# Kernel optimization log

Hardware: AMD Instinct MI355X
Metric: run time of the kernel (lower is better)

## Reference

```python
import jax, jax.numpy as jnp
import numpy as np

EPS = 1e-6
POSE_W, DEPTH_W, POINTS_W, NORMAL_W = 1.0, 1.0, 1.0, 0.1
DEPTH_MIN = 1e-6


def mat_to_quat(M):
    # pytorch3d-style robust rotation-matrix -> quaternion (w,x,y,z)
    m00, m01, m02 = M[..., 0, 0], M[..., 0, 1], M[..., 0, 2]
    m10, m11, m12 = M[..., 1, 0], M[..., 1, 1], M[..., 1, 2]
    m20, m21, m22 = M[..., 2, 0], M[..., 2, 1], M[..., 2, 2]
    q_abs = jnp.sqrt(jnp.maximum(jnp.stack([
        1.0 + m00 + m11 + m22,
        1.0 + m00 - m11 - m22,
        1.0 - m00 + m11 - m22,
        1.0 - m00 - m11 + m22], axis=-1), 0.0))
    cand = jnp.stack([
        jnp.stack([q_abs[..., 0] ** 2, m21 - m12, m02 - m20, m10 - m01], -1),
        jnp.stack([m21 - m12, q_abs[..., 1] ** 2, m10 + m01, m02 + m20], -1),
        jnp.stack([m02 - m20, m10 + m01, q_abs[..., 2] ** 2, m12 + m21], -1),
        jnp.stack([m10 - m01, m20 + m02, m21 + m12, q_abs[..., 3] ** 2], -1),
    ], axis=-2)  # [...,4,4]
    cand = cand / (2.0 * jnp.maximum(q_abs[..., None], 0.1))
    best = jnp.argmax(q_abs, axis=-1)
    quat = jnp.take_along_axis(cand, best[..., None, None], axis=-2)[..., 0, :]
    return jnp.where(quat[..., 0:1] < 0, -quat, quat)


def pose_encoding(extri, intr, H, W):
    # extri [B,S,3,4] -> [B,S,9] = absT(3) + quat(4) + fov_h,fov_w
    T = extri[..., :3, 3]
    quat = mat_to_quat(extri[..., :3, :3])
    fov_h = 2.0 * jnp.arctan((H / 2.0) / intr[..., 1, 1])
    fov_w = 2.0 * jnp.arctan((W / 2.0) / intr[..., 0, 0])
    return jnp.concatenate([T, quat, fov_h[..., None], fov_w[..., None]], axis=-1)


def align_depth_scale(dp, dg, vm):
    # batched masked-median scale; dp detached by caller. Returns (aligned_gt, scales[B,S])
    B, S, H, W = dg.shape
    dpf, dgf = dp.reshape(B, S, H * W), dg.reshape(B, S, H * W)
    m = vm.reshape(B, S, H * W)
    m2 = m & jnp.isfinite(dpf) & (dpf > EPS)
    ratio = dpf / jnp.maximum(dgf, EPS)
    fm = m2 & jnp.isfinite(ratio)
    msum = m2.sum(-1)
    fcnt = fm.sum(-1)
    r = jnp.sort(jnp.where(fm, ratio, jnp.inf), axis=-1)
    idx = jnp.maximum((fcnt - 1) // 2, 0)  # torch lower median
    med = jnp.take_along_axis(r, idx[..., None], axis=-1)[..., 0]
    scale = jnp.clip(med, 1e-3, 1e3)
    scale = jnp.where((msum < 16) | (fcnt == 0), jnp.ones_like(scale), scale)
    return dg * scale[..., None, None], scale


def _cam_grid(depth, intr):
    B, S, H, W = depth.shape
    ys, xs = jnp.meshgrid(jnp.arange(H, dtype=depth.dtype),
                          jnp.arange(W, dtype=depth.dtype), indexing='ij')
    fx = intr[..., 0, 0][..., None, None]
    fy = intr[..., 1, 1][..., None, None]
    cx = intr[..., 0, 2][..., None, None]
    cy = intr[..., 1, 2][..., None, None]
    x = (xs - cx) / jnp.maximum(fx, EPS) * depth
    y = (ys - cy) / jnp.maximum(fy, EPS) * depth
    return jnp.stack([x, y, depth], axis=-1)  # [B,S,H,W,3]


def depth_to_normals(depth, intr):
    pts = _cam_grid(depth, intr)
    fx_diff = pts[..., 1:-1, 2:, :] - pts[..., 1:-1, :-2, :]
    fy_diff = pts[..., 2:, 1:-1, :] - pts[..., :-2, 1:-1, :]
    core = jnp.cross(fy_diff, fx_diff)
    core = core / jnp.maximum(jnp.linalg.norm(core, axis=-1, keepdims=True), EPS)
    return jnp.zeros_like(pts).at[..., 1:-1, 1:-1, :].set(core)


def depth_to_world_points(depth, intr, pose):
    cam_pts = _cam_grid(depth, intr)
    rot = pose[..., :3, :3]
    trans = pose[..., :3, 3]
    return jnp.einsum('bsij,bshwj->bshwi', rot, cam_pts) + trans[..., None, None, :]


def masked_l1(pred, target, mask):
    mask = mask.astype(pred.dtype)
    return ((pred - target) * mask).__abs__().sum() / jnp.maximum(mask.sum(), 1.0)


def masked_cosine_loss(pred, target, mask):
    pred = pred / jnp.maximum(jnp.linalg.norm(pred, axis=-1, keepdims=True), EPS)
    target = target / jnp.maximum(jnp.linalg.norm(target, axis=-1, keepdims=True), EPS)
    cos = jnp.clip((pred * target).sum(-1), -1.0, 1.0)
    m = mask.astype(cos.dtype)
    return ((1.0 - cos) * m).sum() / jnp.maximum(m.sum(), 1.0)


def smooth_l1(pred, target):
    d = jnp.abs(pred - target)
    return jnp.mean(jnp.where(d < 1.0, 0.5 * d * d, d - 0.5))


def supervised_loss(depth_pred, points_pred, pose_pred, depth_gt, intrinsics,
                    pose_matrix_gt, valid_mask):
    B, S, H, W = depth_gt.shape
    vm = valid_mask & jnp.isfinite(depth_gt) & (depth_gt > DEPTH_MIN)
    depth_gt_aligned, scales = align_depth_scale(
        jax.lax.stop_gradient(depth_pred), depth_gt, vm)
    points_gt = depth_to_world_points(depth_gt_aligned, intrinsics, pose_matrix_gt)
    points_mask = jnp.broadcast_to(vm[..., None], points_gt.shape)
    # normal mask: zero-out 1-pixel border
    border = jnp.zeros((H, W), dtype=bool).at[1:-1, 1:-1].set(True)
    normal_mask = vm & border
    pred_normals = depth_to_normals(depth_pred, intrinsics)
    gt_normals = depth_to_normals(depth_gt, intrinsics)
    normal_loss = masked_cosine_loss(pred_normals, gt_normals, normal_mask)
    pose_gt = pose_encoding(pose_matrix_gt[..., :3, :], intrinsics, H, W)
    pose_gt = pose_gt.at[..., :3].multiply(scales[..., None])
    depth_loss = masked_l1(depth_pred, depth_gt_aligned, vm)
    points_loss = masked_l1(points_pred, points_gt, points_mask)
    pose_loss = smooth_l1(pose_pred, pose_gt)
    return (POSE_W * pose_loss + DEPTH_W * depth_loss
            + POINTS_W * points_loss + NORMAL_W * normal_loss)


def setup_inputs() -> dict:
    key = jax.random.key(0)
    ks = jax.random.split(key, 7)
    B, S, H, W = 4, 8, 384, 512
    depth_gt = jax.random.uniform(ks[0], (B, S, H, W), minval=0.5, maxval=10.0)
    depth_pred = depth_gt * jax.random.uniform(ks[1], (B, S, H, W), minval=0.8, maxval=1.2)
    points_pred = jax.random.normal(ks[2], (B, S, H, W, 3))
    pose_pred = 0.1 * jax.random.normal(ks[3], (B, S, 9))
    intr = jnp.broadcast_to(jnp.array([[500.0, 0.0, W / 2.0],
                                       [0.0, 500.0, H / 2.0],
                                       [0.0, 0.0, 1.0]], jnp.float32), (B, S, 3, 3))
    q, _ = jnp.linalg.qr(jax.random.normal(ks[4], (B, S, 3, 3)))
    R = q * jnp.sign(jnp.linalg.det(q))[..., None, None]  # det=+1
    t = jax.random.normal(ks[5], (B, S, 3))
    top = jnp.concatenate([R, t[..., None]], axis=-1)
    bottom = jnp.broadcast_to(jnp.array([0.0, 0.0, 0.0, 1.0], jnp.float32), (B, S, 1, 4))
    pose_matrix_gt = jnp.concatenate([top, bottom], axis=-2)
    valid_mask = jax.random.uniform(ks[6], (B, S, H, W)) > 0.05
    return {"depth_pred": depth_pred, "points_pred": points_pred,
            "pose_pred": pose_pred, "depth_gt": depth_gt,
            "intrinsics": intr, "pose_matrix_gt": pose_matrix_gt,
            "valid_mask": valid_mask}


def reference(depth_pred, points_pred, pose_pred, depth_gt, intrinsics,
              pose_matrix_gt, valid_mask):
    return supervised_loss(depth_pred, points_pred, pose_pred, depth_gt,
                           intrinsics, pose_matrix_gt, valid_mask)
```

## Files before the change

kernel.cpp:

```cpp
#include <hip/hip_runtime.h>
#include <stdint.h>

#define H_ 384
#define W_ 512
#define HW_ (H_ * W_)
#define NIMG 32
#define EPSF 1e-6f
#define HBLK 16
#define HTHR 512
#define PXB (HW_ / HBLK)
#define CITER (PXB / (HTHR * 4))
#define NPARTS (HBLK * NIMG)
#define SENT 0xFFFFFFFFu

#define OFF_MSUM   0
#define OFF_FCNT   32
#define OFF_KREM1  64
#define OFF_PREF1  96
#define OFF_SCALE  128
#define OFF_POSE   160
#define OFF_PMF    192
#define OFF_PART   1216
#define OFF_PHA    3776
#define OFF_PHB    (OFF_PHA + NIMG*HBLK*2048)

__device__ __forceinline__ bool finitef(float x) {
    return ((__float_as_uint(x) >> 23) & 0xFFu) != 0xFFu;
}

__global__ __launch_bounds__(HTHR) void hist0_k(
    const float* __restrict__ dp, const float* __restrict__ dg,
    const uint8_t* __restrict__ vmask, uint32_t* __restrict__ ws)
{
    __shared__ uint32_t lh[2048];
    __shared__ int sm[8], sf[8];
    const int img = blockIdx.y, blk = blockIdx.x, t = threadIdx.x;
    for (int b = t; b < 2048; b += HTHR) lh[b] = 0;
    __syncthreads();

    const size_t base = (size_t)img * HW_;
    const float* dpi = dp + base;
    const float* dgi = dg + base;
    const uint8_t* mi = vmask + base;

    int m2c = 0, fmc = 0;

    for (int c = 0; c < CITER; ++c) {
        const int pix = blk * PXB + c * (HTHR * 4) + t * 4;
        const float4 v_dp = *reinterpret_cast<const float4*>(dpi + pix);
        const float4 v_dg = *reinterpret_cast<const float4*>(dgi + pix);
        const uchar4 v_m  = *reinterpret_cast<const uchar4*>(mi + pix);
        const float dpa[4] = {v_dp.x, v_dp.y, v_dp.z, v_dp.w};
        const float dga[4] = {v_dg.x, v_dg.y, v_dg.z, v_dg.w};
        const uint8_t ma[4] = {v_m.x, v_m.y, v_m.z, v_m.w};
        int bins[4]; bool fms[4];
#pragma unroll
        for (int e = 0; e < 4; ++e) {
            const float dgv = dga[e], dpv = dpa[e];
            const bool vm = ma[e] && finitef(dgv) && (dgv > 1e-6f);
            const bool m2 = vm && finitef(dpv) && (dpv > EPSF);
            const float ratio = dpv / fmaxf(dgv, EPSF);
            const bool fm = m2 && finitef(ratio);
            m2c += (int)m2; fmc += (int)fm;
            const uint32_t key = fm ? __float_as_uint(ratio) : SENT;
            bins[e] = (int)(key >> 21);
            fms[e] = fm;
        }

#pragma unroll
        for (int e = 0; e < 4; ++e) {
            const bool fm = fms[e];
            const int bin = bins[e];
            unsigned long long todo = __ballot(fm);
            while (todo) {
                const int lead = (int)__ffsll(todo) - 1;
                const int lbin = __shfl(bin, lead);
                const unsigned long long same = __ballot(fm && (bin == lbin));
                if ((t & 63) == lead)
                    atomicAdd(&lh[lbin], (uint32_t)__popcll(same));
                todo &= ~same;
            }
        }
    }

    for (int o = 32; o > 0; o >>= 1) { m2c += __shfl_down(m2c, o); fmc += __shfl_down(fmc, o); }
    if ((t & 63) == 0) { sm[t >> 6] = m2c; sf[t >> 6] = fmc; }
    __syncthreads();
    if (t == 0) {
        int M = 0, F = 0;
        for (int w = 0; w < 8; ++w) { M += sm[w]; F += sf[w]; }
        int* pmf = (int*)(ws + OFF_PMF) + (img * HBLK + blk) * 2;
        pmf[0] = M; pmf[1] = F;
    }

    uint32_t* phb = ws + OFF_PHA + (size_t)(img * HBLK + blk) * 2048;
    for (int b = t; b < 2048; b += HTHR) phb[b] = lh[b];
}

__global__ __launch_bounds__(HTHR) void histp1_k(
    const float* __restrict__ dp, const float* __restrict__ dg,
    const uint8_t* __restrict__ vmask, uint32_t* __restrict__ ws)
{
    __shared__ uint32_t lh[2048];
    __shared__ uint32_t wsum[8];
    __shared__ int s_bin, s_krem, s_msum, s_fcnt;
    const int img = blockIdx.y, blk = blockIdx.x, t = threadIdx.x;

    const uint32_t* pin = ws + OFF_PHA + (size_t)img * HBLK * 2048;
    uint32_t local[4];
#pragma unroll
    for (int c = 0; c < 4; ++c) local[c] = 0;
    for (int b = 0; b < HBLK; ++b) {
        const uint32_t* row = pin + b * 2048 + t * 4;
#pragma unroll
        for (int c = 0; c < 4; ++c) local[c] += row[c];
    }
    const uint32_t cs = local[0] + local[1] + local[2] + local[3];

    uint32_t v = cs;
#pragma unroll
    for (int o = 1; o < 64; o <<= 1) {
        const uint32_t u = __shfl_up(v, o);
        if ((t & 63) >= o) v += u;
    }
    if ((t & 63) == 63) wsum[t >> 6] = v;
    if (t == 0) {
        s_bin = 0; s_krem = 0;
        const int* pmf = (const int*)(ws + OFF_PMF) + img * HBLK * 2;
        int M = 0, F = 0;
        for (int b = 0; b < HBLK; ++b) { M += pmf[2 * b]; F += pmf[2 * b + 1]; }
        s_msum = M; s_fcnt = F;
    }
    __syncthreads();
    uint32_t woff = 0;
    for (int w = 0; w < (t >> 6); ++w) woff += wsum[w];
    const uint32_t incl = woff + v;
    const uint32_t excl = incl - cs;

    const uint32_t k = (uint32_t)max((s_fcnt - 1) / 2, 0);
    if (k >= excl && k < incl) {
        uint32_t cum = excl;
#pragma unroll
        for (int c = 0; c < 4; ++c) {
            if (cum + local[c] > k) { s_bin = t * 4 + c; s_krem = (int)(k - cum); break; }
            cum += local[c];
        }
    }
    __syncthreads();
    if (t == 0 && blk == 0) {
        ((int*)(ws + OFF_MSUM))[img] = s_msum;
        ((int*)(ws + OFF_FCNT))[img] = s_fcnt;
        (ws + OFF_PREF1)[img] = (uint32_t)s_bin << 21;
        ((int*)(ws + OFF_KREM1))[img] = s_krem;
    }
    const uint32_t pm = (uint32_t)s_bin;

    for (int b = t; b < 2048; b += HTHR) lh[b] = 0;
    __syncthreads();

    const size_t base = (size_t)img * HW_;
    for (int c = 0; c < CITER; ++c) {
        const int pix = blk * PXB + c * (HTHR * 4) + t * 4;
        const float4 v_dp = *reinterpret_cast<const float4*>(dp + base + pix);
        const float4 v_dg = *reinterpret_cast<const float4*>(dg + base + pix);
        const uchar4 v_m  = *reinterpret_cast<const uchar4*>(vmask + base + pix);
        const float dpa[4] = {v_dp.x, v_dp.y, v_dp.z, v_dp.w};
        const float dga[4] = {v_dg.x, v_dg.y, v_dg.z, v_dg.w};
        const uint8_t ma[4] = {v_m.x, v_m.y, v_m.z, v_m.w};
#pragma unroll
        for (int e = 0; e < 4; ++e) {
            const float dgv = dga[e], dpv = dpa[e];
            const bool vm = ma[e] && finitef(dgv) && (dgv > 1e-6f);
            const bool m2 = vm && finitef(dpv) && (dpv > EPSF);
            const float ratio = dpv / fmaxf(dgv, EPSF);
            const bool fm = m2 && finitef(ratio);
            const uint32_t key = fm ? __float_as_uint(ratio) : SENT;
            if ((key >> 21) == pm)
                atomicAdd(&lh[(key >> 10) & 2047u], 1u);
        }
    }
    __syncthreads();

    uint32_t* pout = ws + OFF_PHB + (size_t)(img * HBLK + blk) * 2048;
    for (int b = t; b < 2048; b += HTHR) pout[b] = lh[b];
}

__global__ __launch_bounds__(256) void sel_mid_k(
    uint32_t* __restrict__ ws,
    const float* __restrict__ intr, const float* __restrict__ posegt,
    const float* __restrict__ posepred)
{
    const int img = blockIdx.x;
    const int t = threadIdx.x;
    const uint32_t* ph = ws + OFF_PHB + (size_t)img * HBLK * 2048;
    uint32_t local[8];
#pragma unroll
    for (int c = 0; c < 8; ++c) local[c] = 0;
    for (int b = 0; b < HBLK; ++b) {
        const uint32_t* row = ph + b * 2048 + t * 8;
#pragma unroll
        for (int c = 0; c < 8; ++c) local[c] += row[c];
    }
    uint32_t cs = 0;
#pragma unroll
    for (int c = 0; c < 8; ++c) cs += local[c];

    __shared__ uint32_t wsum[4];
    __shared__ int s_bin;
    uint32_t v = cs;
#pragma unroll
    for (int o = 1; o < 64; o <<= 1) {
        const uint32_t u = __shfl_up(v, o);
        if ((t & 63) >= o) v += u;
    }
    if ((t & 63) == 63) wsum[t >> 6] = v;
    if (t == 0) s_bin = 0;
    __syncthreads();
    uint32_t woff = 0;
    for (int w = 0; w < (t >> 6); ++w) woff += wsum[w];
    const uint32_t incl = woff + v;
    const uint32_t excl = incl - cs;

    const uint32_t k = (uint32_t)((const int*)(ws + OFF_KREM1))[img];
    if (k >= excl && k < incl) {
        uint32_t cum = excl;
#pragma unroll
        for (int c = 0; c < 8; ++c) {
            if (cum + local[c] > k) { s_bin = t * 8 + c; break; }
            cum += local[c];
        }
    }
    __syncthreads();

    if (t == 0) {
        const uint32_t med_u = (ws + OFF_PREF1)[img] | ((uint32_t)s_bin << 10) | 512u;
        const float med = __uint_as_float(med_u);
        float sc_ = fminf(fmaxf(med, 0.001f), 1000.0f);
        const int fcnt = ((const int*)(ws + OFF_FCNT))[img];
        const int msum = ((const int*)(ws + OFF_MSUM))[img];
        if (msum < 16 || fcnt == 0) sc_ = 1.0f;
        ((float*)(ws + OFF_SCALE))[img] = sc_;

        const float* p = posegt + img * 16;
        const float m00 = p[0], m01 = p[1], m02 = p[2], tx = p[3];
        const float m10 = p[4], m11 = p[5], m12 = p[6], ty = p[7];
        const float m20 = p[8], m21 = p[9], m22 = p[10], tz = p[11];
        float qa[4];
        qa[0] = sqrtf(fmaxf(1.0f + m00 + m11 + m22, 0.0f));
        qa[1] = sqrtf(fmaxf(1.0f + m00 - m11 - m22, 0.0f));
        qa[2] = sqrtf(fmaxf(1.0f - m00 + m11 - m22, 0.0f));
        qa[3] = sqrtf(fmaxf(1.0f - m00 - m11 + m22, 0.0f));
        int best = 0; float bv = qa[0];
        for (int i2 = 1; i2 < 4; ++i2) if (qa[i2] > bv) { bv = qa[i2]; best = i2; }
        float c0, c1, c2, c3;
        if (best == 0)      { c0 = qa[0]*qa[0]; c1 = m21 - m12;   c2 = m02 - m20;   c3 = m10 - m01; }
        else if (best == 1) { c0 = m21 - m12;   c1 = qa[1]*qa[1]; c2 = m10 + m01;   c3 = m02 + m20; }
        else if (best == 2) { c0 = m02 - m20;   c1 = m10 + m01;   c2 = qa[2]*qa[2]; c3 = m12 + m21; }
        else                { c0 = m10 - m01;   c1 = m20 + m02;   c2 = m21 + m12;   c3 = qa[3]*qa[3]; }
        const float denom = 2.0f * fmaxf(qa[best], 0.1f);
        float q0 = c0 / denom, q1 = c1 / denom, q2 = c2 / denom, q3 = c3 / denom;
        if (q0 < 0.0f) { q0 = -q0; q1 = -q1; q2 = -q2; q3 = -q3; }
        const float fx = intr[img * 9 + 0], fy = intr[img * 9 + 4];
        const float fovh = 2.0f * atanf((H_ * 0.5f) / fy);
        const float fovw = 2.0f * atanf((W_ * 0.5f) / fx);
        const float pg[9] = {tx * sc_, ty * sc_, tz * sc_, q0, q1, q2, q3, fovh, fovw};
        const float* ppred = posepred + img * 9;
        float s = 0.0f;
        for (int i2 = 0; i2 < 9; ++i2) {
            const float d = fabsf(ppred[i2] - pg[i2]);
            s += (d < 1.0f) ? 0.5f * d * d : d - 0.5f;
        }
        ((float*)(ws + OFF_POSE))[img] = s;
    }
}

__global__ __launch_bounds__(HTHR) void main_loss(
    const float* __restrict__ dp, const float* __restrict__ dg,
    const uint8_t* __restrict__ vmask, const float* __restrict__ pts_pred,
    const float* __restrict__ intr, const float* __restrict__ posegt,
    uint32_t* __restrict__ ws)
{
    const int img = blockIdx.y, blk = blockIdx.x, t = threadIdx.x;
    __shared__ float sP[17];
    if (t == 0) {
        const float* p = posegt + img * 16;
        sP[0] = p[0]; sP[1] = p[1]; sP[2] = p[2];  sP[9]  = p[3];
        sP[3] = p[4]; sP[4] = p[5]; sP[5] = p[6];  sP[10] = p[7];
        sP[6] = p[8]; sP[7] = p[9]; sP[8] = p[10]; sP[11] = p[11];
        sP[12] = intr[img * 9 + 0]; sP[13] = intr[img * 9 + 4];
        sP[14] = intr[img * 9 + 2]; sP[15] = intr[img * 9 + 5];
        sP[16] = ((const float*)(ws + OFF_SCALE))[img];
    }
    __syncthreads();
    const float R00 = sP[0], R01 = sP[1], R02 = sP[2];
    const float R10 = sP[3], R11 = sP[4], R12 = sP[5];
    const float R20 = sP[6], R21 = sP[7], R22 = sP[8];
    const float T0 = sP[9], T1 = sP[10], T2 = sP[11];
    const float inv_fx = 1.0f / fmaxf(sP[12], EPSF);
    const float inv_fy = 1.0f / fmaxf(sP[13], EPSF);
    const float cx = sP[14], cy = sP[15];
    const float sc = sP[16];

    const size_t base = (size_t)img * HW_;
    const float* dpi = dp + base;
    const float* dgi = dg + base;

    float dsum = 0.0f, psum = 0.0f, nsum = 0.0f;
    float vcnt = 0.0f, ncnt = 0.0f;

    for (int c = 0; c < CITER; ++c) {
        const int pix = blk * PXB + c * (HTHR * 4) + t * 4;
        const int i = pix >> 9;
        const int j0 = pix & 511;

        const float4 v_dp = *reinterpret_cast<const float4*>(dpi + pix);
        const float4 v_dg = *reinterpret_cast<const float4*>(dgi + pix);
        const uchar4 v_m  = *reinterpret_cast<const uchar4*>(vmask + base + pix);
        const float4 pp0 = *reinterpret_cast<const float4*>(pts_pred + (base + pix) * 3);
        const float4 pp1 = *reinterpret_cast<const float4*>(pts_pred + (base + pix) * 3 + 4);
        const float4 pp2 = *reinterpret_cast<const float4*>(pts_pred + (base + pix) * 3 + 8);

        const int im = (i > 0) ? i - 1 : 0;
        const int ip = (i < H_ - 1) ? i + 1 : i;
        const int jme = (j0 > 0) ? j0 - 1 : 0;
        const int jpe = (j0 + 4 < W_) ? j0 + 4 : W_ - 1;
        const float4 dpU = *reinterpret_cast<const float4*>(dpi + im * W_ + j0);
        const float4 dpD = *reinterpret_cast<const float4*>(dpi + ip * W_ + j0);
        const float4 dgU = *reinterpret_cast<const float4*>(dgi + im * W_ + j0);
        const float4 dgD = *reinterpret_cast<const float4*>(dgi + ip * W_ + j0);
        const float dpLe = dpi[i * W_ + jme], dpRe = dpi[i * W_ + jpe];
        const float dgLe = dgi[i * W_ + jme], dgRe = dgi[i * W_ + jpe];

        const float ppv[12] = {pp0.x, pp0.y, pp0.z, pp0.w, pp1.x, pp1.y, pp1.z, pp1.w,
                               pp2.x, pp2.y, pp2.z, pp2.w};
        const float dpa[4] = {v_dp.x, v_dp.y, v_dp.z, v_dp.w};
        const float dga[4] = {v_dg.x, v_dg.y, v_dg.z, v_dg.w};
        const float dpUa[4] = {dpU.x, dpU.y, dpU.z, dpU.w};
        const float dpDa[4] = {dpD.x, dpD.y, dpD.z, dpD.w};
        const float dgUa[4] = {dgU.x, dgU.y, dgU.z, dgU.w};
        const float dgDa[4] = {dgD.x, dgD.y, dgD.z, dgD.w};
        const uint8_t ma[4] = {v_m.x, v_m.y, v_m.z, v_m.w};

        const float ay = ((float)i - cy) * inv_fy;
        const bool row_int = (i >= 1) && (i <= H_ - 2);

#pragma unroll
        for (int e = 0; e < 4; ++e) {
            const int j = j0 + e;
            const float dgv = dga[e], dpv = dpa[e];
            const bool vm = ma[e] && finitef(dgv) && (dgv > 1e-6f);
            const bool nm = vm && row_int && (j >= 1) && (j <= W_ - 2);
            vcnt += vm ? 1.0f : 0.0f;
            ncnt += nm ? 1.0f : 0.0f;

            const float dal = dgv * sc;
            dsum += vm ? fabsf(dpv - dal) : 0.0f;
            const float ax = ((float)j - cx) * inv_fx;
            const float cxx = ax * dal, cyy = ay * dal;
            const float wx = R00 * cxx + R01 * cyy + R02 * dal + T0;
            const float wy = R10 * cxx + R11 * cyy + R12 * dal + T1;
            const float wz = R20 * cxx + R21 * cyy + R22 * dal + T2;
            const float pl = fabsf(ppv[3 * e] - wx) + fabsf(ppv[3 * e + 1] - wy)
                           + fabsf(ppv[3 * e + 2] - wz);
            psum += vm ? pl : 0.0f;

            const float pdL = (e == 0) ? dpLe : dpa[e - 1];
            const float pdR = (e == 3) ? dpRe : dpa[e + 1];
            const float gdL = (e == 0) ? dgLe : dga[e - 1];
            const float gdR = (e == 3) ? dgRe : dga[e + 1];
            const float pdU = dpUa[e], pdD = dpDa[e];
            const float gdU = dgUa[e], gdD = dgDa[e];

            const float dRLp = pdR - pdL, dDUp = pdD - pdU;
            const float Ap = inv_fy * (pdD + pdU);
            const float Bp = inv_fx * (pdR + pdL);
            const float cpx = dRLp * Ap;
            const float cpy = dDUp * Bp;
            const float cpz = -(Ap * Bp + ax * cpx + ay * cpy);
            const float dRLg = gdR - gdL, dDUg = gdD - gdU;
            const float Ag = inv_fy * (gdD + gdU);
            const float Bg = inv_fx * (gdR + gdL);
            const float cgx = dRLg * Ag;
            const float cgy = dDUg * Bg;
            const float cgz = -(Ag * Bg + ax * cgx + ay * cgy);

            const float np2 = cpx * cpx + cpy * cpy + cpz * cpz;
            const float ng2 = cgx * cgx + cgy * cgy + cgz * cgz;
            const float dpg = cpx * cgx + cpy * cgy + cpz * cgz;
            const float den = fmaxf(np2, 1e-12f) * fmaxf(ng2, 1e-12f);
            float cosv = dpg * __builtin_amdgcn_rsqf(den);
            cosv = fminf(fmaxf(cosv, -1.0f), 1.0f);
            nsum += nm ? (1.0f - cosv) : 0.0f;
        }
    }

    float vals[5] = {vcnt, dsum, psum, nsum, ncnt};
    __shared__ float red[8][5];
    const int wave = t >> 6, lane = t & 63;
#pragma unroll
    for (int q = 0; q < 5; ++q) {
        float v = vals[q];
        for (int o = 32; o > 0; o >>= 1) v += __shfl_down(v, o);
        if (lane == 0) red[wave][q] = v;
    }
    __syncthreads();
    if (t == 0) {
        const int slot = img * HBLK + blk;
        float* part = (float*)(ws + OFF_PART) + slot * 5;
#pragma unroll
        for (int q = 0; q < 5; ++q) {
            float s = 0.0f;
            for (int w = 0; w < 8; ++w) s += red[w][q];
            part[q] = s;
        }
    }
}

__global__ __launch_bounds__(256) void finalize_k(const uint32_t* __restrict__ ws,
                                                  float* __restrict__ out)
{
    const float* part = (const float*)(ws + OFF_PART);
    const int t = threadIdx.x;
    double s[5] = {0, 0, 0, 0, 0};
    for (int slot = t; slot < NPARTS; slot += 256) {
#pragma unroll
        for (int q = 0; q < 5; ++q) s[q] += (double)part[slot * 5 + q];
    }
    __shared__ double red[4][5];
    const int wave = t >> 6, lane = t & 63;
#pragma unroll
    for (int q = 0; q < 5; ++q) {
        double v = s[q];
        for (int o = 32; o > 0; o >>= 1) v += __shfl_down(v, o);
        if (lane == 0) red[wave][q] = v;
    }
    __syncthreads();
    if (t == 0) {
        double tot[5];
#pragma unroll
        for (int q = 0; q < 5; ++q)
            tot[q] = red[0][q] + red[1][q] + red[2][q] + red[3][q];
        const float* pose = (const float*)(ws + OFF_POSE);
        double ps = 0.0;
        for (int i2 = 0; i2 < NIMG; ++i2) ps += (double)pose[i2];
        const double vmc = tot[0];
        const double depth_loss  = tot[1] / fmax(vmc, 1.0);
        const double points_loss = tot[2] / fmax(3.0 * vmc, 1.0);
        const double normal_loss = tot[3] / fmax(tot[4], 1.0);
        const double pose_loss   = ps / 288.0;
        out[0] = (float)(pose_loss + depth_loss + points_loss + 0.1 * normal_loss);
    }
}

extern "C" void kernel_launch(void* const* d_in, const int* in_sizes, int n_in,
                              void* d_out, int out_size, void* d_ws, size_t ws_size,
                              hipStream_t stream)
{
    const float*   dp       = (const float*)d_in[0];
    const float*   pts_pred = (const float*)d_in[1];
    const float*   posepred = (const float*)d_in[2];
    const float*   dg       = (const float*)d_in[3];
    const float*   intr     = (const float*)d_in[4];
    const float*   posegt   = (const float*)d_in[5];
    const uint8_t* vmask    = (const uint8_t*)d_in[6];
    float* out = (float*)d_out;
    uint32_t* ws = (uint32_t*)d_ws;

    const dim3 hgrid(HBLK, NIMG);
    hist0_k<<<hgrid, HTHR, 0, stream>>>(dp, dg, vmask, ws);
    histp1_k<<<hgrid, HTHR, 0, stream>>>(dp, dg, vmask, ws);
    sel_mid_k<<<NIMG, 256, 0, stream>>>(ws, intr, posegt, posepred);
    main_loss<<<hgrid, HTHR, 0, stream>>>(dp, dg, vmask, pts_pred, intr, posegt, ws);
    finalize_k<<<1, 256, 0, stream>>>(ws, out);
}
```

Before: 62.76 us.

## Fold median-select and pose loss into main loss kernel, coarsen second histogram

Removes the separate selection kernel by having each main_loss block redundantly reduce the per-image partial histograms and pick the median bin. Block 0 of each image also computes the pose loss. The second-pass histogram shrinks from 2048 to 256 bins, so the median is resolved to 13 low mantissa bits instead of 10. That cuts one launch and the histogram traffic, but the scale is now approximated to a coarser midpoint, which may change results slightly.

Result: faster. 59.04 us (-5.9%).

```diff
diff --git a/kernel.cpp b/kernel.cpp
--- a/kernel.cpp
+++ b/kernel.cpp
@@ -17,11 +17,10 @@
 #define OFF_FCNT   32
 #define OFF_KREM1  64
 #define OFF_PREF1  96
-#define OFF_SCALE  128
-#define OFF_POSE   160
-#define OFF_PMF    192
-#define OFF_PART   1216
-#define OFF_PHA    3776
+#define OFF_POSE   128
+#define OFF_PMF    160
+#define OFF_PART   1184
+#define OFF_PHA    3744
 #define OFF_PHB    (OFF_PHA + NIMG*HBLK*2048)
 
 __device__ __forceinline__ bool finitef(float x) {
@@ -155,7 +154,7 @@
     }
     const uint32_t pm = (uint32_t)s_bin;
 
-    for (int b = t; b < 2048; b += HTHR) lh[b] = 0;
+    if (t < 256) lh[t] = 0;
     __syncthreads();
 
     const size_t base = (size_t)img * HW_;
@@ -176,120 +175,97 @@
             const bool fm = m2 && finitef(ratio);
             const uint32_t key = fm ? __float_as_uint(ratio) : SENT;
             if ((key >> 21) == pm)
-                atomicAdd(&lh[(key >> 10) & 2047u], 1u);
-        }
-    }
-    __syncthreads();
-
-    uint32_t* pout = ws + OFF_PHB + (size_t)(img * HBLK + blk) * 2048;
-    for (int b = t; b < 2048; b += HTHR) pout[b] = lh[b];
-}
-
-__global__ __launch_bounds__(256) void sel_mid_k(
-    uint32_t* __restrict__ ws,
-    const float* __restrict__ intr, const float* __restrict__ posegt,
-    const float* __restrict__ posepred)
-{
-    const int img = blockIdx.x;
-    const int t = threadIdx.x;
-    const uint32_t* ph = ws + OFF_PHB + (size_t)img * HBLK * 2048;
-    uint32_t local[8];
-#pragma unroll
-    for (int c = 0; c < 8; ++c) local[c] = 0;
-    for (int b = 0; b < HBLK; ++b) {
-        const uint32_t* row = ph + b * 2048 + t * 8;
-#pragma unroll
-        for (int c = 0; c < 8; ++c) local[c] += row[c];
-    }
-    uint32_t cs = 0;
-#pragma unroll
-    for (int c = 0; c < 8; ++c) cs += local[c];
-
-    __shared__ uint32_t wsum[4];
-    __shared__ int s_bin;
-    uint32_t v = cs;
-#pragma unroll
-    for (int o = 1; o < 64; o <<= 1) {
-        const uint32_t u = __shfl_up(v, o);
-        if ((t & 63) >= o) v += u;
-    }
-    if ((t & 63) == 63) wsum[t >> 6] = v;
-    if (t == 0) s_bin = 0;
-    __syncthreads();
-    uint32_t woff = 0;
-    for (int w = 0; w < (t >> 6); ++w) woff += wsum[w];
-    const uint32_t incl = woff + v;
-    const uint32_t excl = incl - cs;
-
-    const uint32_t k = (uint32_t)((const int*)(ws + OFF_KREM1))[img];
-    if (k >= excl && k < incl) {
-        uint32_t cum = excl;
-#pragma unroll
-        for (int c = 0; c < 8; ++c) {
-            if (cum + local[c] > k) { s_bin = t * 8 + c; break; }
-            cum += local[c];
-        }
-    }
-    __syncthreads();
-
-    if (t == 0) {
-        const uint32_t med_u = (ws + OFF_PREF1)[img] | ((uint32_t)s_bin << 10) | 512u;
-        const float med = __uint_as_float(med_u);
-        float sc_ = fminf(fmaxf(med, 0.001f), 1000.0f);
-        const int fcnt = ((const int*)(ws + OFF_FCNT))[img];
-        const int msum = ((const int*)(ws + OFF_MSUM))[img];
-        if (msum < 16 || fcnt == 0) sc_ = 1.0f;
-        ((float*)(ws + OFF_SCALE))[img] = sc_;
-
-        const float* p = posegt + img * 16;
-        const float m00 = p[0], m01 = p[1], m02 = p[2], tx = p[3];
-        const float m10 = p[4], m11 = p[5], m12 = p[6], ty = p[7];
-        const float m20 = p[8], m21 = p[9], m22 = p[10], tz = p[11];
-        float qa[4];
-        qa[0] = sqrtf(fmaxf(1.0f + m00 + m11 + m22, 0.0f));
-        qa[1] = sqrtf(fmaxf(1.0f + m00 - m11 - m22, 0.0f));
-        qa[2] = sqrtf(fmaxf(1.0f - m00 + m11 - m22, 0.0f));
-        qa[3] = sqrtf(fmaxf(1.0f - m00 - m11 + m22, 0.0f));
-        int best = 0; float bv = qa[0];
-        for (int i2 = 1; i2 < 4; ++i2) if (qa[i2] > bv) { bv = qa[i2]; best = i2; }
-        float c0, c1, c2, c3;
-        if (best == 0)      { c0 = qa[0]*qa[0]; c1 = m21 - m12;   c2 = m02 - m20;   c3 = m10 - m01; }
-        else if (best == 1) { c0 = m21 - m12;   c1 = qa[1]*qa[1]; c2 = m10 + m01;   c3 = m02 + m20; }
-        else if (best == 2) { c0 = m02 - m20;   c1 = m10 + m01;   c2 = qa[2]*qa[2]; c3 = m12 + m21; }
-        else                { c0 = m10 - m01;   c1 = m20 + m02;   c2 = m21 + m12;   c3 = qa[3]*qa[3]; }
-        const float denom = 2.0f * fmaxf(qa[best], 0.1f);
-        float q0 = c0 / denom, q1 = c1 / denom, q2 = c2 / denom, q3 = c3 / denom;
-        if (q0 < 0.0f) { q0 = -q0; q1 = -q1; q2 = -q2; q3 = -q3; }
-        const float fx = intr[img * 9 + 0], fy = intr[img * 9 + 4];
-        const float fovh = 2.0f * atanf((H_ * 0.5f) / fy);
-        const float fovw = 2.0f * atanf((W_ * 0.5f) / fx);
-        const float pg[9] = {tx * sc_, ty * sc_, tz * sc_, q0, q1, q2, q3, fovh, fovw};
-        const float* ppred = posepred + img * 9;
-        float s = 0.0f;
-        for (int i2 = 0; i2 < 9; ++i2) {
-            const float d = fabsf(ppred[i2] - pg[i2]);
-            s += (d < 1.0f) ? 0.5f * d * d : d - 0.5f;
-        }
-        ((float*)(ws + OFF_POSE))[img] = s;
-    }
+                atomicAdd(&lh[(key >> 13) & 255u], 1u);
+        }
+    }
+    __syncthreads();
+
+    uint32_t* pout = ws + OFF_PHB + (size_t)(img * HBLK + blk) * 256;
+    if (t < 256) pout[t] = lh[t];
 }
 
 __global__ __launch_bounds__(HTHR) void main_loss(
     const float* __restrict__ dp, const float* __restrict__ dg,
     const uint8_t* __restrict__ vmask, const float* __restrict__ pts_pred,
     const float* __restrict__ intr, const float* __restrict__ posegt,
-    uint32_t* __restrict__ ws)
+    const float* __restrict__ posepred, uint32_t* __restrict__ ws)
 {
     const int img = blockIdx.y, blk = blockIdx.x, t = threadIdx.x;
     __shared__ float sP[17];
+    __shared__ uint32_t wsum[4];
+    __shared__ int s_bin;
+
+    {
+        uint32_t cs = 0, vscan = 0;
+        if (t < 256) {
+            const uint32_t* ph = ws + OFF_PHB + (size_t)img * HBLK * 256;
+            for (int b = 0; b < HBLK; ++b) cs += ph[b * 256 + t];
+            uint32_t v = cs;
+#pragma unroll
+            for (int o = 1; o < 64; o <<= 1) {
+                const uint32_t u = __shfl_up(v, o);
+                if ((t & 63) >= o) v += u;
+            }
+            vscan = v;
+            if ((t & 63) == 63) wsum[t >> 6] = v;
+        }
+        if (t == 0) s_bin = 0;
+        __syncthreads();
+        if (t < 256) {
+            uint32_t woff = 0;
+            for (int w = 0; w < (t >> 6); ++w) woff += wsum[w];
+            const uint32_t incl = woff + vscan;
+            const uint32_t excl = incl - cs;
+            const uint32_t k = (uint32_t)((const int*)(ws + OFF_KREM1))[img];
+            if (k >= excl && k < incl) s_bin = t;
+        }
+        __syncthreads();
+    }
     if (t == 0) {
+        const uint32_t med_u = (ws + OFF_PREF1)[img] | ((uint32_t)s_bin << 13) | 4096u;
+        float sc_ = fminf(fmaxf(__uint_as_float(med_u), 0.001f), 1000.0f);
+        const int fcnt = ((const int*)(ws + OFF_FCNT))[img];
+        const int msum = ((const int*)(ws + OFF_MSUM))[img];
+        if (msum < 16 || fcnt == 0) sc_ = 1.0f;
+
         const float* p = posegt + img * 16;
         sP[0] = p[0]; sP[1] = p[1]; sP[2] = p[2];  sP[9]  = p[3];
         sP[3] = p[4]; sP[4] = p[5]; sP[5] = p[6];  sP[10] = p[7];
         sP[6] = p[8]; sP[7] = p[9]; sP[8] = p[10]; sP[11] = p[11];
         sP[12] = intr[img * 9 + 0]; sP[13] = intr[img * 9 + 4];
         sP[14] = intr[img * 9 + 2]; sP[15] = intr[img * 9 + 5];
-        sP[16] = ((const float*)(ws + OFF_SCALE))[img];
+        sP[16] = sc_;
+
+        if (blk == 0) {
+            const float m00 = p[0], m01 = p[1], m02 = p[2], tx = p[3];
+            const float m10 = p[4], m11 = p[5], m12 = p[6], ty = p[7];
+            const float m20 = p[8], m21 = p[9], m22 = p[10], tz = p[11];
+            float qa[4];
+            qa[0] = sqrtf(fmaxf(1.0f + m00 + m11 + m22, 0.0f));
+            qa[1] = sqrtf(fmaxf(1.0f + m00 - m11 - m22, 0.0f));
+            qa[2] = sqrtf(fmaxf(1.0f - m00 + m11 - m22, 0.0f));
+            qa[3] = sqrtf(fmaxf(1.0f - m00 - m11 + m22, 0.0f));
+            int best = 0; float bv = qa[0];
+            for (int i2 = 1; i2 < 4; ++i2) if (qa[i2] > bv) { bv = qa[i2]; best = i2; }
+            float c0, c1, c2, c3;
+            if (best == 0)      { c0 = qa[0]*qa[0]; c1 = m21 - m12;   c2 = m02 - m20;   c3 = m10 - m01; }
+            else if (best == 1) { c0 = m21 - m12;   c1 = qa[1]*qa[1]; c2 = m10 + m01;   c3 = m02 + m20; }
+            else if (best == 2) { c0 = m02 - m20;   c1 = m10 + m01;   c2 = qa[2]*qa[2]; c3 = m12 + m21; }
+            else                { c0 = m10 - m01;   c1 = m20 + m02;   c2 = m21 + m12;   c3 = qa[3]*qa[3]; }
+            const float denom = 2.0f * fmaxf(qa[best], 0.1f);
+            float q0 = c0 / denom, q1 = c1 / denom, q2 = c2 / denom, q3 = c3 / denom;
+            if (q0 < 0.0f) { q0 = -q0; q1 = -q1; q2 = -q2; q3 = -q3; }
+            const float fovh = 2.0f * atanf((H_ * 0.5f) / sP[13]);
+            const float fovw = 2.0f * atanf((W_ * 0.5f) / sP[12]);
+            const float pg[9] = {tx * sc_, ty * sc_, tz * sc_, q0, q1, q2, q3, fovh, fovw};
+            const float* ppred = posepred + img * 9;
+            float s = 0.0f;
+            for (int i2 = 0; i2 < 9; ++i2) {
+                const float d = fabsf(ppred[i2] - pg[i2]);
+                s += (d < 1.0f) ? 0.5f * d * d : d - 0.5f;
+            }
+            ((float*)(ws + OFF_POSE))[img] = s;
+        }
     }
     __syncthreads();
     const float R00 = sP[0], R01 = sP[1], R02 = sP[2];
@@ -469,7 +445,6 @@
     const dim3 hgrid(HBLK, NIMG);
     hist0_k<<<hgrid, HTHR, 0, stream>>>(dp, dg, vmask, ws);
     histp1_k<<<hgrid, HTHR, 0, stream>>>(dp, dg, vmask, ws);
-    sel_mid_k<<<NIMG, 256, 0, stream>>>(ws, intr, posegt, posepred);
-    main_loss<<<hgrid, HTHR, 0, stream>>>(dp, dg, vmask, pts_pred, intr, posegt, ws);
+    main_loss<<<hgrid, HTHR, 0, stream>>>(dp, dg, vmask, pts_pred, intr, posegt, posepred, ws);
     finalize_k<<<1, 256, 0, stream>>>(ws, out);
 }
```
